# Optimization experiments

Hardware: AMD Instinct MI355X
Metric: run time of the kernel (lower is better)

The kernel has to match this reference:

```python
import jax, jax.numpy as jnp
import numpy as np

N, F_IN, H, C = 100000, 256, 128, 64
E, EP = 1600000, 500000


def setup_inputs() -> dict:
    key = jax.random.key(0)
    ks = jax.random.split(key, 8)
    x = jax.random.normal(ks[0], (N, F_IN), jnp.float32)
    masked_nodes = jax.random.randint(ks[1], (1000,), 0, N)
    pos_edge_index = jax.random.randint(ks[2], (2, EP), 0, N)
    neg_edge_index = jax.random.randint(ks[3], (2, EP), 0, N)
    edge_index = jax.random.randint(ks[4], (2, E), 0, N)
    W1 = jax.random.normal(ks[5], (F_IN, H), jnp.float32) / np.sqrt(F_IN).astype(np.float32)
    b1 = jnp.zeros((H,), jnp.float32)
    W2 = jax.random.normal(ks[6], (H, C), jnp.float32) / np.sqrt(H).astype(np.float32)
    b2 = jnp.zeros((C,), jnp.float32)
    return dict(x=x, masked_nodes=masked_nodes, pos_edge_index=pos_edge_index,
                neg_edge_index=neg_edge_index, edge_index=edge_index,
                W1=W1, b1=b1, W2=W2, b2=b2)


def gcn_conv(x, W, b, src, dst, n):
    # PyG GCNConv: h = x @ W; symmetric norm with self-loops; aggregate; + bias
    h = x @ W  # [N, out]
    deg = jax.ops.segment_sum(jnp.ones(src.shape[0], h.dtype), dst, num_segments=n) + 1.0
    dis = jax.lax.rsqrt(deg)  # D^{-1/2} including self-loop
    msg = h[src] * (dis[src] * dis[dst])[:, None]           # gather + edge-norm
    agg = jax.ops.segment_sum(msg, dst, num_segments=n)      # scatter-add
    agg = agg + h * (dis * dis)[:, None]                      # self-loop term
    return agg + b


def reference(x, masked_nodes, pos_edge_index, neg_edge_index, edge_index, W1, b1, W2, b2):
    n = x.shape[0]
    src, dst = edge_index[0], edge_index[1]
    h = jax.nn.relu(gcn_conv(x, W1, b1, src, dst, n))
    h = gcn_conv(h, W2, b2, src, dst, n)  # [N, C]
    tei = jnp.concatenate([pos_edge_index, neg_edge_index], axis=-1)  # [2, 2*EP]
    x_j = h[tei[0]]  # [2EP, C]
    x_i = h[tei[1]]
    scores = jnp.einsum('ef,ef->e', x_i, x_j)
    return scores, jnp.zeros(tei.shape, jnp.float32)
```

## Files before the change

kernel.cpp:

```cpp
#include <hip/hip_runtime.h>

#define N_NODES 100000
#define F_IN    256
#define H_DIM   128
#define C_DIM   64
#define E_EDGES 1600000
#define EP_EDGES 500000

#define NBUK 391
#define EPB  4096

typedef unsigned short bf16_t;
typedef short  short8  __attribute__((ext_vector_type(8)));
typedef float  float4v __attribute__((ext_vector_type(4)));

__device__ inline bf16_t f2bf(float f) {
    unsigned u = __float_as_uint(f);
    u += 0x7fff + ((u >> 16) & 1);
    return (bf16_t)(u >> 16);
}
__device__ inline float bf2f(bf16_t h) {
    return __uint_as_float(((unsigned)h) << 16);
}
__device__ inline void split8(const float* vv, short* h, short* l) {
#pragma unroll
    for (int j = 0; j < 8; ++j) {
        bf16_t hb = f2bf(vv[j]);
        h[j] = (short)hb;
        l[j] = (short)f2bf(vv[j] - bf2f(hb));
    }
}
__device__ inline float4v mfma16(short8 a, short8 b, float4v c) {
    return __builtin_amdgcn_mfma_f32_16x16x32_bf16(a, b, c, 0, 0, 0);
}

__global__ __launch_bounds__(256) void bhist_kernel(const int* __restrict__ dst,
                                                    int* __restrict__ bsize) {
    __shared__ int hist[NBUK];
    const int t = threadIdx.x;
    for (int b = t; b < NBUK; b += 256) hist[b] = 0;
    __syncthreads();
    const int e0 = blockIdx.x * EPB;
#pragma unroll
    for (int i = 0; i < 16; ++i) {
        int e = e0 + i * 256 + t;
        if (e < E_EDGES) atomicAdd(&hist[dst[e] >> 8], 1);
    }
    __syncthreads();
    for (int b = t; b < NBUK; b += 256)
        if (hist[b]) atomicAdd(&bsize[b], hist[b]);
}

__global__ __launch_bounds__(512) void bscan_kernel(const int* __restrict__ bsize,
                                                    int* __restrict__ bbase,
                                                    int* __restrict__ bcursor) {
    __shared__ int sh[512];
    int t = threadIdx.x;
    sh[t] = (t < NBUK) ? bsize[t] : 0;
    __syncthreads();
#pragma unroll
    for (int off = 1; off < 512; off <<= 1) {
        int u = (t >= off) ? sh[t - off] : 0;
        __syncthreads();
        sh[t] += u;
        __syncthreads();
    }
    if (t < NBUK) {
        int ex = (t == 0) ? 0 : sh[t - 1];
        bbase[t] = ex;
        bcursor[t] = ex;
    }
    if (t == 0) bbase[NBUK] = E_EDGES;
}

__global__ __launch_bounds__(256) void bucket_scatter_kernel(const int* __restrict__ src,
                                                             const int* __restrict__ dst,
                                                             int* __restrict__ bcursor,
                                                             int2* __restrict__ pairs) {
    __shared__ int hist[NBUK];
    __shared__ int base[NBUK];
    const int t = threadIdx.x;
    for (int b = t; b < NBUK; b += 256) hist[b] = 0;
    __syncthreads();

    const int e0 = blockIdx.x * EPB;
    int s[16], d[16];
#pragma unroll
    for (int i = 0; i < 16; ++i) {
        int e = e0 + i * 256 + t;
        if (e < E_EDGES) {
            s[i] = src[e];
            d[i] = dst[e];
            atomicAdd(&hist[d[i] >> 8], 1);
        } else {
            d[i] = -1;
        }
    }
    __syncthreads();
    for (int b = t; b < NBUK; b += 256) {
        int c = hist[b];
        base[b] = c ? atomicAdd(&bcursor[b], c) : 0;
        hist[b] = 0;
    }
    __syncthreads();
#pragma unroll
    for (int i = 0; i < 16; ++i) {
        if (d[i] >= 0) {
            int b = d[i] >> 8;
            int r = atomicAdd(&hist[b], 1);
            pairs[base[b] + r] = make_int2(s[i], d[i]);
        }
    }
}

__global__ __launch_bounds__(256) void bucket_sort_kernel(const int2* __restrict__ pairs,
                                                          const int* __restrict__ bbase,
                                                          int* __restrict__ row_ptr,
                                                          float* __restrict__ dis,
                                                          int* __restrict__ csr_src) {
    __shared__ int cnt[256];
    __shared__ int sh[256];
    __shared__ int cur[256];
    const int b = blockIdx.x;
    const int node0 = b << 8;
    const int t = threadIdx.x;
    const int nn = min(256, N_NODES - node0);
    const int beg = bbase[b], end = bbase[b + 1];
    cnt[t] = 0;
    __syncthreads();
    for (int e = beg + t; e < end; e += 256)
        atomicAdd(&cnt[pairs[e].y - node0], 1);
    __syncthreads();
    int c = cnt[t];
    if (t < nn) dis[node0 + t] = rsqrtf((float)c + 1.0f);
    sh[t] = c;
    __syncthreads();
#pragma unroll
    for (int off = 1; off < 256; off <<= 1) {
        int u = (t >= off) ? sh[t - off] : 0;
        __syncthreads();
        sh[t] += u;
        __syncthreads();
    }
    int start = beg + sh[t] - c;
    if (t < nn) row_ptr[node0 + t] = start;
    cur[t] = start;
    if (b == NBUK - 1 && t == 0) row_ptr[N_NODES] = E_EDGES;
    __syncthreads();
    for (int e = beg + t; e < end; e += 256) {
        int2 p = pairs[e];
        int j = atomicAdd(&cur[p.y - node0], 1);
        csr_src[j] = p.x;
    }
}

__global__ __launch_bounds__(256) void wprep_kernel(const float* __restrict__ W1,
                                                    const float* __restrict__ W2,
                                                    short* __restrict__ w1h,
                                                    short* __restrict__ w1l,
                                                    short* __restrict__ w2h,
                                                    short* __restrict__ w2l) {
    int idx = blockIdx.x * 256 + threadIdx.x;
    if (idx < H_DIM * F_IN) {
        int n = idx >> 8, k = idx & 255;
        float w = W1[k * H_DIM + n];
        bf16_t h = f2bf(w);
        w1h[idx] = (short)h;
        w1l[idx] = (short)f2bf(w - bf2f(h));
    }
    int i2 = idx - H_DIM * F_IN;
    if (i2 >= 0 && i2 < C_DIM * H_DIM) {
        int n = i2 >> 7, k = i2 & 127;
        float w = W2[k * C_DIM + n];
        bf16_t h = f2bf(w);
        w2h[i2] = (short)h;
        w2l[i2] = (short)f2bf(w - bf2f(h));
    }
}

#define LSTR 40
__global__ __launch_bounds__(256) void gemm1_mfma(const float* __restrict__ X,
                                                  const short* __restrict__ Wth,
                                                  const short* __restrict__ Wtl,
                                                  bf16_t* __restrict__ T,
                                                  int nrows) {
    __shared__ short Ah[128 * LSTR], Al[128 * LSTR];
    __shared__ short Bh[128 * LSTR], Bl[128 * LSTR];
    const int t = threadIdx.x;
    const int row0 = blockIdx.x * 128;
    const int w = t >> 6;
    const int lane = t & 63;
    const int m = lane & 15;
    const int q = lane >> 4;
    const int koff = q * 8;

    float4v acc[2][8];
#pragma unroll
    for (int i = 0; i < 2; ++i)
#pragma unroll
        for (int j = 0; j < 8; ++j) acc[i][j] = {0.f, 0.f, 0.f, 0.f};

    for (int ks = 0; ks < 8; ++ks) {
        const int k0 = ks * 32;
#pragma unroll
        for (int i = 0; i < 2; ++i) {
            int c = t + i * 256;
            int r = c >> 2, kc = c & 3;
            int row = row0 + r;
            float vv[8] = {0.f, 0.f, 0.f, 0.f, 0.f, 0.f, 0.f, 0.f};
            if (row < nrows) {
                float4 v0 = *(const float4*)&X[(long long)row * F_IN + k0 + kc * 8];
                float4 v1 = *(const float4*)&X[(long long)row * F_IN + k0 + kc * 8 + 4];
                vv[0] = v0.x; vv[1] = v0.y; vv[2] = v0.z; vv[3] = v0.w;
                vv[4] = v1.x; vv[5] = v1.y; vv[6] = v1.z; vv[7] = v1.w;
            }
            short h[8], l[8];
            split8(vv, h, l);
            *(short8*)&Ah[r * LSTR + kc * 8] = *(short8*)h;
            *(short8*)&Al[r * LSTR + kc * 8] = *(short8*)l;
        }
#pragma unroll
        for (int i = 0; i < 2; ++i) {
            int c = t + i * 256;
            int n = c >> 2, kc = c & 3;
            *(short8*)&Bh[n * LSTR + kc * 8] = *(const short8*)&Wth[n * F_IN + k0 + kc * 8];
            *(short8*)&Bl[n * LSTR + kc * 8] = *(const short8*)&Wtl[n * F_IN + k0 + kc * 8];
        }
        __syncthreads();

        short8 ah0 = *(const short8*)&Ah[(w * 32 + m) * LSTR + koff];
        short8 ah1 = *(const short8*)&Ah[(w * 32 + 16 + m) * LSTR + koff];
        short8 al0 = *(const short8*)&Al[(w * 32 + m) * LSTR + koff];
        short8 al1 = *(const short8*)&Al[(w * 32 + 16 + m) * LSTR + koff];
#pragma unroll
        for (int nc = 0; nc < 8; ++nc) {
            short8 bh = *(const short8*)&Bh[(nc * 16 + m) * LSTR + koff];
            short8 bl = *(const short8*)&Bl[(nc * 16 + m) * LSTR + koff];
            acc[0][nc] = mfma16(ah0, bh, acc[0][nc]);
            acc[0][nc] = mfma16(al0, bh, acc[0][nc]);
            acc[0][nc] = mfma16(ah0, bl, acc[0][nc]);
            acc[1][nc] = mfma16(ah1, bh, acc[1][nc]);
            acc[1][nc] = mfma16(al1, bh, acc[1][nc]);
            acc[1][nc] = mfma16(ah1, bl, acc[1][nc]);
        }
        __syncthreads();
    }
#pragma unroll
    for (int mt = 0; mt < 2; ++mt)
#pragma unroll
        for (int nc = 0; nc < 8; ++nc)
#pragma unroll
            for (int reg = 0; reg < 4; ++reg) {
                int grow = row0 + w * 32 + mt * 16 + q * 4 + reg;
                int gcol = nc * 16 + m;
                if (grow < nrows)
                    T[(long long)grow * H_DIM + gcol] = f2bf(acc[mt][nc][reg]);
            }
}

__global__ __launch_bounds__(256) void gemm2_mfma(const float* __restrict__ A,
                                                  const float* __restrict__ b1,
                                                  const short* __restrict__ Wth,
                                                  const short* __restrict__ Wtl,
                                                  bf16_t* __restrict__ T,
                                                  int nrows) {
    __shared__ short Ah[128 * LSTR], Al[128 * LSTR];
    __shared__ short Bh[64 * LSTR], Bl[64 * LSTR];
    const int t = threadIdx.x;
    const int row0 = blockIdx.x * 128;
    const int w = t >> 6;
    const int lane = t & 63;
    const int m = lane & 15;
    const int q = lane >> 4;
    const int koff = q * 8;

    float4v acc[2][4];
#pragma unroll
    for (int i = 0; i < 2; ++i)
#pragma unroll
        for (int j = 0; j < 4; ++j) acc[i][j] = {0.f, 0.f, 0.f, 0.f};

    for (int ks = 0; ks < 4; ++ks) {
        const int k0 = ks * 32;
#pragma unroll
        for (int i = 0; i < 2; ++i) {
            int c = t + i * 256;
            int r = c >> 2, kc = c & 3;
            int row = row0 + r;
            float vv[8] = {0.f, 0.f, 0.f, 0.f, 0.f, 0.f, 0.f, 0.f};
            if (row < nrows) {
                float4 v0 = *(const float4*)&A[(long long)row * H_DIM + k0 + kc * 8];
                float4 v1 = *(const float4*)&A[(long long)row * H_DIM + k0 + kc * 8 + 4];
                float4 b0 = *(const float4*)&b1[k0 + kc * 8];
                float4 b1v = *(const float4*)&b1[k0 + kc * 8 + 4];
                vv[0] = fmaxf(v0.x + b0.x, 0.f);  vv[1] = fmaxf(v0.y + b0.y, 0.f);
                vv[2] = fmaxf(v0.z + b0.z, 0.f);  vv[3] = fmaxf(v0.w + b0.w, 0.f);
                vv[4] = fmaxf(v1.x + b1v.x, 0.f); vv[5] = fmaxf(v1.y + b1v.y, 0.f);
                vv[6] = fmaxf(v1.z + b1v.z, 0.f); vv[7] = fmaxf(v1.w + b1v.w, 0.f);
            }
            short h[8], l[8];
            split8(vv, h, l);
            *(short8*)&Ah[r * LSTR + kc * 8] = *(short8*)h;
            *(short8*)&Al[r * LSTR + kc * 8] = *(short8*)l;
        }
        {
            int n = t >> 2, kc = t & 3;
            *(short8*)&Bh[n * LSTR + kc * 8] = *(const short8*)&Wth[n * H_DIM + k0 + kc * 8];
            *(short8*)&Bl[n * LSTR + kc * 8] = *(const short8*)&Wtl[n * H_DIM + k0 + kc * 8];
        }
        __syncthreads();

        short8 ah0 = *(const short8*)&Ah[(w * 32 + m) * LSTR + koff];
        short8 ah1 = *(const short8*)&Ah[(w * 32 + 16 + m) * LSTR + koff];
        short8 al0 = *(const short8*)&Al[(w * 32 + m) * LSTR + koff];
        short8 al1 = *(const short8*)&Al[(w * 32 + 16 + m) * LSTR + koff];
#pragma unroll
        for (int nc = 0; nc < 4; ++nc) {
            short8 bh = *(const short8*)&Bh[(nc * 16 + m) * LSTR + koff];
            short8 bl = *(const short8*)&Bl[(nc * 16 + m) * LSTR + koff];
            acc[0][nc] = mfma16(ah0, bh, acc[0][nc]);
            acc[0][nc] = mfma16(al0, bh, acc[0][nc]);
            acc[0][nc] = mfma16(ah0, bl, acc[0][nc]);
            acc[1][nc] = mfma16(ah1, bh, acc[1][nc]);
            acc[1][nc] = mfma16(al1, bh, acc[1][nc]);
            acc[1][nc] = mfma16(ah1, bl, acc[1][nc]);
        }
        __syncthreads();
    }
#pragma unroll
    for (int mt = 0; mt < 2; ++mt)
#pragma unroll
        for (int nc = 0; nc < 4; ++nc)
#pragma unroll
            for (int reg = 0; reg < 4; ++reg) {
                int grow = row0 + w * 32 + mt * 16 + q * 4 + reg;
                int gcol = nc * 16 + m;
                if (grow < nrows)
                    T[(long long)grow * C_DIM + gcol] = f2bf(acc[mt][nc][reg]);
            }
}

__device__ inline void fma8_bf16(float* acc, uint4 u, float c) {
#pragma unroll
    for (int p = 0; p < 4; ++p) {
        unsigned w = (&u.x)[p];
        float lo = __uint_as_float(w << 16);
        float hi = __uint_as_float(w & 0xffff0000u);
        acc[2 * p]     = fmaf(lo, c, acc[2 * p]);
        acc[2 * p + 1] = fmaf(hi, c, acc[2 * p + 1]);
    }
}

template <int CS, bool HAS_BIAS>
__global__ __launch_bounds__(256) void agg_kernel(const bf16_t* __restrict__ t,
                                                  const float* __restrict__ dis,
                                                  const int* __restrict__ row_ptr,
                                                  const int* __restrict__ csr_src,
                                                  const float* __restrict__ bias,
                                                  float* __restrict__ agg) {
    unsigned idx = blockIdx.x * 256u + threadIdx.x;
    if (idx >= (unsigned)(N_NODES << CS)) return;
    int node = idx >> CS;
    int q = idx & ((1 << CS) - 1);
    const uint4* tv = (const uint4*)t;
    float dd = dis[node];
    int beg = row_ptr[node], end = row_ptr[node + 1];

    float acc[8];
#pragma unroll
    for (int p = 0; p < 8; ++p) acc[p] = 0.0f;
    fma8_bf16(acc, tv[idx], dd * dd);

    int j = beg;
    for (; j + 3 < end; j += 4) {
        int s0 = csr_src[j + 0], s1 = csr_src[j + 1];
        int s2 = csr_src[j + 2], s3 = csr_src[j + 3];
        float c0 = dis[s0] * dd, c1 = dis[s1] * dd;
        float c2 = dis[s2] * dd, c3 = dis[s3] * dd;
        uint4 u0 = tv[((unsigned)s0 << CS) + q];
        uint4 u1 = tv[((unsigned)s1 << CS) + q];
        uint4 u2 = tv[((unsigned)s2 << CS) + q];
        uint4 u3 = tv[((unsigned)s3 << CS) + q];
        fma8_bf16(acc, u0, c0);
        fma8_bf16(acc, u1, c1);
        fma8_bf16(acc, u2, c2);
        fma8_bf16(acc, u3, c3);
    }
    for (; j < end; ++j) {
        int s = csr_src[j];
        float c = dis[s] * dd;
        fma8_bf16(acc, tv[((unsigned)s << CS) + q], c);
    }

    if (HAS_BIAS) {
        float4 bv0 = ((const float4*)bias)[q * 2];
        float4 bv1 = ((const float4*)bias)[q * 2 + 1];
        acc[0] += bv0.x; acc[1] += bv0.y; acc[2] += bv0.z; acc[3] += bv0.w;
        acc[4] += bv1.x; acc[5] += bv1.y; acc[6] += bv1.z; acc[7] += bv1.w;
    }
    float4 o0 = make_float4(acc[0], acc[1], acc[2], acc[3]);
    float4 o1 = make_float4(acc[4], acc[5], acc[6], acc[7]);
    ((float4*)agg)[idx * 2]     = o0;
    ((float4*)agg)[idx * 2 + 1] = o1;
}

__global__ __launch_bounds__(256) void score_kernel(const float* __restrict__ h2,
                                                    const int* __restrict__ pos,
                                                    const int* __restrict__ neg,
                                                    float* __restrict__ out) {
    int tid = blockIdx.x * 256 + threadIdx.x;
    int e = tid >> 4;
    int q = tid & 15;
    if (e >= 2 * EP_EDGES) return;
    int i, j;
    if (e < EP_EDGES) {
        j = pos[e];
        i = pos[EP_EDGES + e];
    } else {
        j = neg[e - EP_EDGES];
        i = neg[e];
    }
    float4 a = ((const float4*)h2)[i * (C_DIM / 4) + q];
    float4 b = ((const float4*)h2)[j * (C_DIM / 4) + q];
    float v = a.x * b.x + a.y * b.y + a.z * b.z + a.w * b.w;
    v += __shfl_down(v, 8, 16);
    v += __shfl_down(v, 4, 16);
    v += __shfl_down(v, 2, 16);
    v += __shfl_down(v, 1, 16);
    if (q == 0) out[e] = v;
}

extern "C" void kernel_launch(void* const* d_in, const int* in_sizes, int n_in,
                              void* d_out, int out_size, void* d_ws, size_t ws_size,
                              hipStream_t stream) {
    const float* x  = (const float*)d_in[0];
    const int* pos  = (const int*)d_in[2];
    const int* neg  = (const int*)d_in[3];
    const int* ei   = (const int*)d_in[4];
    const float* W1 = (const float*)d_in[5];
    const float* b1 = (const float*)d_in[6];
    const float* W2 = (const float*)d_in[7];
    const float* b2 = (const float*)d_in[8];
    float* out = (float*)d_out;

    char* ws = (char*)d_ws;
    float*  dis     = (float*) (ws + 0);
    int*    row_ptr = (int*)   (ws + 400000);
    int*    bsize   = (int*)   (ws + 800128);
    int*    bbase   = (int*)   (ws + 801792);
    int*    bcursor = (int*)   (ws + 803456);
    int*    csr_src = (int*)   (ws + 805120);
    int2*   pairs   = (int2*)  (ws + 7205120);
    bf16_t* t       = (bf16_t*)(ws + 20005120);
    float*  agg     = (float*) (ws + 45605120);
    short*  w1th    = (short*) (ws + 96805120);
    short*  w1tl    = (short*) (ws + 96870656);
    short*  w2th    = (short*) (ws + 96936192);
    short*  w2tl    = (short*) (ws + 96952576);

    const int* esrc = ei;
    const int* edst = ei + E_EDGES;

    hipMemsetAsync(bsize, 0, NBUK * sizeof(int), stream);
    bhist_kernel<<<(E_EDGES + EPB - 1) / EPB, 256, 0, stream>>>(edst, bsize);
    bscan_kernel<<<1, 512, 0, stream>>>(bsize, bbase, bcursor);
    bucket_scatter_kernel<<<(E_EDGES + EPB - 1) / EPB, 256, 0, stream>>>(
        esrc, edst, bcursor, pairs);
    bucket_sort_kernel<<<NBUK, 256, 0, stream>>>(pairs, bbase, row_ptr, dis, csr_src);
    wprep_kernel<<<(H_DIM * F_IN + C_DIM * H_DIM + 255) / 256, 256, 0, stream>>>(
        W1, W2, w1th, w1tl, w2th, w2tl);

    gemm1_mfma<<<(N_NODES + 127) / 128, 256, 0, stream>>>(x, w1th, w1tl, t, N_NODES);
    agg_kernel<4, false><<<(N_NODES * 16 + 255) / 256, 256, 0, stream>>>(
        t, dis, row_ptr, csr_src, nullptr, agg);

    gemm2_mfma<<<(N_NODES + 127) / 128, 256, 0, stream>>>(agg, b1, w2th, w2tl, t, N_NODES);
    agg_kernel<3, true><<<(N_NODES * 8 + 255) / 256, 256, 0, stream>>>(
        t, dis, row_ptr, csr_src, b2, agg);

    score_kernel<<<(2 * EP_EDGES * 16) / 256, 256, 0, stream>>>(agg, pos, neg, out);

    hipMemsetAsync(out + 2 * EP_EDGES, 0, (size_t)4 * EP_EDGES * sizeof(float), stream);
}
```

Before: 438.8 us.

## Load GEMM operands directly into MFMA registers, dropping LDS staging and barriers

Both GEMM kernels now have each lane load its own A-row fragment straight from global memory and split it to bf16 hi/lo in registers. Each lane also reads the pre-split weight fragments directly from global memory. This removes the shared-memory tiles and the two __syncthreads per k-step, and the k-loop is fully unrolled. In exchange, every wave re-reads the whole weight matrix through cache, and the A loads are strided per lane (8 floats per row) rather than cooperatively coalesced.

```diff
diff --git a/kernel.cpp b/kernel.cpp
--- a/kernel.cpp
+++ b/kernel.cpp
@@ -22,12 +22,12 @@
 __device__ inline float bf2f(bf16_t h) {
     return __uint_as_float(((unsigned)h) << 16);
 }
-__device__ inline void split8(const float* vv, short* h, short* l) {
+__device__ inline void split8(const float* vv, short8* h, short8* l) {
 #pragma unroll
     for (int j = 0; j < 8; ++j) {
         bf16_t hb = f2bf(vv[j]);
-        h[j] = (short)hb;
-        l[j] = (short)f2bf(vv[j] - bf2f(hb));
+        (*h)[j] = (short)hb;
+        (*l)[j] = (short)f2bf(vv[j] - bf2f(hb));
     }
 }
 __device__ inline float4v mfma16(short8 a, short8 b, float4v c) {
@@ -178,21 +178,23 @@
     }
 }
 
-#define LSTR 40
 __global__ __launch_bounds__(256) void gemm1_mfma(const float* __restrict__ X,
                                                   const short* __restrict__ Wth,
                                                   const short* __restrict__ Wtl,
                                                   bf16_t* __restrict__ T,
                                                   int nrows) {
-    __shared__ short Ah[128 * LSTR], Al[128 * LSTR];
-    __shared__ short Bh[128 * LSTR], Bl[128 * LSTR];
     const int t = threadIdx.x;
     const int row0 = blockIdx.x * 128;
     const int w = t >> 6;
     const int lane = t & 63;
     const int m = lane & 15;
     const int q = lane >> 4;
-    const int koff = q * 8;
+
+    const int r0 = row0 + w * 32 + m;
+    const int r1 = r0 + 16;
+    const bool ok0 = r0 < nrows, ok1 = r1 < nrows;
+    const float* pa0 = X + (long long)r0 * F_IN + q * 8;
+    const float* pa1 = X + (long long)r1 * F_IN + q * 8;
 
     float4v acc[2][8];
 #pragma unroll
@@ -200,42 +202,31 @@
 #pragma unroll
         for (int j = 0; j < 8; ++j) acc[i][j] = {0.f, 0.f, 0.f, 0.f};
 
+#pragma unroll
     for (int ks = 0; ks < 8; ++ks) {
         const int k0 = ks * 32;
-#pragma unroll
-        for (int i = 0; i < 2; ++i) {
-            int c = t + i * 256;
-            int r = c >> 2, kc = c & 3;
-            int row = row0 + r;
-            float vv[8] = {0.f, 0.f, 0.f, 0.f, 0.f, 0.f, 0.f, 0.f};
-            if (row < nrows) {
-                float4 v0 = *(const float4*)&X[(long long)row * F_IN + k0 + kc * 8];
-                float4 v1 = *(const float4*)&X[(long long)row * F_IN + k0 + kc * 8 + 4];
-                vv[0] = v0.x; vv[1] = v0.y; vv[2] = v0.z; vv[3] = v0.w;
-                vv[4] = v1.x; vv[5] = v1.y; vv[6] = v1.z; vv[7] = v1.w;
-            }
-            short h[8], l[8];
-            split8(vv, h, l);
-            *(short8*)&Ah[r * LSTR + kc * 8] = *(short8*)h;
-            *(short8*)&Al[r * LSTR + kc * 8] = *(short8*)l;
-        }
-#pragma unroll
-        for (int i = 0; i < 2; ++i) {
-            int c = t + i * 256;
-            int n = c >> 2, kc = c & 3;
-            *(short8*)&Bh[n * LSTR + kc * 8] = *(const short8*)&Wth[n * F_IN + k0 + kc * 8];
-            *(short8*)&Bl[n * LSTR + kc * 8] = *(const short8*)&Wtl[n * F_IN + k0 + kc * 8];
-        }
-        __syncthreads();
-
-        short8 ah0 = *(const short8*)&Ah[(w * 32 + m) * LSTR + koff];
-        short8 ah1 = *(const short8*)&Ah[(w * 32 + 16 + m) * LSTR + koff];
-        short8 al0 = *(const short8*)&Al[(w * 32 + m) * LSTR + koff];
-        short8 al1 = *(const short8*)&Al[(w * 32 + 16 + m) * LSTR + koff];
+        float a0f[8] = {0,0,0,0,0,0,0,0}, a1f[8] = {0,0,0,0,0,0,0,0};
+        if (ok0) {
+            float4 u0 = *(const float4*)(pa0 + k0);
+            float4 u1 = *(const float4*)(pa0 + k0 + 4);
+            a0f[0]=u0.x; a0f[1]=u0.y; a0f[2]=u0.z; a0f[3]=u0.w;
+            a0f[4]=u1.x; a0f[5]=u1.y; a0f[6]=u1.z; a0f[7]=u1.w;
+        }
+        if (ok1) {
+            float4 u0 = *(const float4*)(pa1 + k0);
+            float4 u1 = *(const float4*)(pa1 + k0 + 4);
+            a1f[0]=u0.x; a1f[1]=u0.y; a1f[2]=u0.z; a1f[3]=u0.w;
+            a1f[4]=u1.x; a1f[5]=u1.y; a1f[6]=u1.z; a1f[7]=u1.w;
+        }
+        short8 ah0, al0, ah1, al1;
+        split8(a0f, &ah0, &al0);
+        split8(a1f, &ah1, &al1);
+        const int kb = k0 + q * 8;
 #pragma unroll
         for (int nc = 0; nc < 8; ++nc) {
-            short8 bh = *(const short8*)&Bh[(nc * 16 + m) * LSTR + koff];
-            short8 bl = *(const short8*)&Bl[(nc * 16 + m) * LSTR + koff];
+            const int n = nc * 16 + m;
+            short8 bh = *(const short8*)&Wth[n * F_IN + kb];
+            short8 bl = *(const short8*)&Wtl[n * F_IN + kb];
             acc[0][nc] = mfma16(ah0, bh, acc[0][nc]);
             acc[0][nc] = mfma16(al0, bh, acc[0][nc]);
             acc[0][nc] = mfma16(ah0, bl, acc[0][nc]);
@@ -243,7 +234,6 @@
             acc[1][nc] = mfma16(al1, bh, acc[1][nc]);
             acc[1][nc] = mfma16(ah1, bl, acc[1][nc]);
         }
-        __syncthreads();
     }
 #pragma unroll
     for (int mt = 0; mt < 2; ++mt)
@@ -264,15 +254,18 @@
                                                   const short* __restrict__ Wtl,
                                                   bf16_t* __restrict__ T,
                                                   int nrows) {
-    __shared__ short Ah[128 * LSTR], Al[128 * LSTR];
-    __shared__ short Bh[64 * LSTR], Bl[64 * LSTR];
     const int t = threadIdx.x;
     const int row0 = blockIdx.x * 128;
     const int w = t >> 6;
     const int lane = t & 63;
     const int m = lane & 15;
     const int q = lane >> 4;
-    const int koff = q * 8;
+
+    const int r0 = row0 + w * 32 + m;
+    const int r1 = r0 + 16;
+    const bool ok0 = r0 < nrows, ok1 = r1 < nrows;
+    const float* pa0 = A + (long long)r0 * H_DIM + q * 8;
+    const float* pa1 = A + (long long)r1 * H_DIM + q * 8;
 
     float4v acc[2][4];
 #pragma unroll
@@ -280,44 +273,42 @@
 #pragma unroll
         for (int j = 0; j < 4; ++j) acc[i][j] = {0.f, 0.f, 0.f, 0.f};
 
+#pragma unroll
     for (int ks = 0; ks < 4; ++ks) {
         const int k0 = ks * 32;
-#pragma unroll
-        for (int i = 0; i < 2; ++i) {
-            int c = t + i * 256;
-            int r = c >> 2, kc = c & 3;
-            int row = row0 + r;
-            float vv[8] = {0.f, 0.f, 0.f, 0.f, 0.f, 0.f, 0.f, 0.f};
-            if (row < nrows) {
-                float4 v0 = *(const float4*)&A[(long long)row * H_DIM + k0 + kc * 8];
-                float4 v1 = *(const float4*)&A[(long long)row * H_DIM + k0 + kc * 8 + 4];
-                float4 b0 = *(const float4*)&b1[k0 + kc * 8];
-                float4 b1v = *(const float4*)&b1[k0 + kc * 8 + 4];
-                vv[0] = fmaxf(v0.x + b0.x, 0.f);  vv[1] = fmaxf(v0.y + b0.y, 0.f);
-                vv[2] = fmaxf(v0.z + b0.z, 0.f);  vv[3] = fmaxf(v0.w + b0.w, 0.f);
-                vv[4] = fmaxf(v1.x + b1v.x, 0.f); vv[5] = fmaxf(v1.y + b1v.y, 0.f);
-                vv[6] = fmaxf(v1.z + b1v.z, 0.f); vv[7] = fmaxf(v1.w + b1v.w, 0.f);
-            }
-            short h[8], l[8];
-            split8(vv, h, l);
-            *(short8*)&Ah[r * LSTR + kc * 8] = *(short8*)h;
-            *(short8*)&Al[r * LSTR + kc * 8] = *(short8*)l;
-        }
+        float bb[8];
         {
-            int n = t >> 2, kc = t & 3;
-            *(short8*)&Bh[n * LSTR + kc * 8] = *(const short8*)&Wth[n * H_DIM + k0 + kc * 8];
-            *(short8*)&Bl[n * LSTR + kc * 8] = *(const short8*)&Wtl[n * H_DIM + k0 + kc * 8];
-        }
-        __syncthreads();
-
-        short8 ah0 = *(const short8*)&Ah[(w * 32 + m) * LSTR + koff];
-        short8 ah1 = *(const short8*)&Ah[(w * 32 + 16 + m) * LSTR + koff];
-        short8 al0 = *(const short8*)&Al[(w * 32 + m) * LSTR + koff];
-        short8 al1 = *(const short8*)&Al[(w * 32 + 16 + m) * LSTR + koff];
+            float4 u0 = *(const float4*)&b1[k0 + q * 8];
+            float4 u1 = *(const float4*)&b1[k0 + q * 8 + 4];
+            bb[0]=u0.x; bb[1]=u0.y; bb[2]=u0.z; bb[3]=u0.w;
+            bb[4]=u1.x; bb[5]=u1.y; bb[6]=u1.z; bb[7]=u1.w;
+        }
+        float a0f[8] = {0,0,0,0,0,0,0,0}, a1f[8] = {0,0,0,0,0,0,0,0};
+        if (ok0) {
+            float4 u0 = *(const float4*)(pa0 + k0);
+            float4 u1 = *(const float4*)(pa0 + k0 + 4);
+            a0f[0]=fmaxf(u0.x+bb[0],0.f); a0f[1]=fmaxf(u0.y+bb[1],0.f);
+            a0f[2]=fmaxf(u0.z+bb[2],0.f); a0f[3]=fmaxf(u0.w+bb[3],0.f);
+            a0f[4]=fmaxf(u1.x+bb[4],0.f); a0f[5]=fmaxf(u1.y+bb[5],0.f);
+            a0f[6]=fmaxf(u1.z+bb[6],0.f); a0f[7]=fmaxf(u1.w+bb[7],0.f);
+        }
+        if (ok1) {
+            float4 u0 = *(const float4*)(pa1 + k0);
+            float4 u1 = *(const float4*)(pa1 + k0 + 4);
+            a1f[0]=fmaxf(u0.x+bb[0],0.f); a1f[1]=fmaxf(u0.y+bb[1],0.f);
+            a1f[2]=fmaxf(u0.z+bb[2],0.f); a1f[3]=fmaxf(u0.w+bb[3],0.f);
+            a1f[4]=fmaxf(u1.x+bb[4],0.f); a1f[5]=fmaxf(u1.y+bb[5],0.f);
+            a1f[6]=fmaxf(u1.z+bb[6],0.f); a1f[7]=fmaxf(u1.w+bb[7],0.f);
+        }
+        short8 ah0, al0, ah1, al1;
+        split8(a0f, &ah0, &al0);
+        split8(a1f, &ah1, &al1);
+        const int kb = k0 + q * 8;
 #pragma unroll
         for (int nc = 0; nc < 4; ++nc) {
-            short8 bh = *(const short8*)&Bh[(nc * 16 + m) * LSTR + koff];
-            short8 bl = *(const short8*)&Bl[(nc * 16 + m) * LSTR + koff];
+            const int n = nc * 16 + m;
+            short8 bh = *(const short8*)&Wth[n * H_DIM + kb];
+            short8 bl = *(const short8*)&Wtl[n * H_DIM + kb];
             acc[0][nc] = mfma16(ah0, bh, acc[0][nc]);
             acc[0][nc] = mfma16(al0, bh, acc[0][nc]);
             acc[0][nc] = mfma16(ah0, bl, acc[0][nc]);
@@ -325,7 +316,6 @@
             acc[1][nc] = mfma16(al1, bh, acc[1][nc]);
             acc[1][nc] = mfma16(ah1, bl, acc[1][nc]);
         }
-        __syncthreads();
     }
 #pragma unroll
     for (int mt = 0; mt < 2; ++mt)
```

Result: slower. 476.6 us (+8.6%).
